# Performance work log

Measured on AMD Instinct MI355X. Metric: run time of the kernel, lower is better.

## Reference

```python
import jax, jax.numpy as jnp
import numpy as np

VOC = 50000; E = 300; HE = 512; HO = 1024; TN = 5; A = 256; L = 100; T = 48; B = 32
DIN = E + HO + E  # 1624 decoder lstm input
HD = HO           # decoder hidden size


def lstm_cell(x, h, c, Wih, Whh, b):
    g = x @ Wih.T + h @ Whh.T + b
    i, f, gg, o = jnp.split(g, 4, axis=-1)  # torch gate order i,f,g,o
    c2 = jax.nn.sigmoid(f) * c + jax.nn.sigmoid(i) * jnp.tanh(gg)
    h2 = jax.nn.sigmoid(o) * jnp.tanh(c2)
    return h2, c2


def run_lstm(xs, Wih, Whh, b, H):
    # xs: [S, B, E] seq-first
    h0 = jnp.zeros((xs.shape[1], H), xs.dtype)
    def step(carry, x):
        h, c = carry
        h2, c2 = lstm_cell(x, h, c, Wih, Whh, b)
        return (h2, c2), h2
    (h, c), ys = jax.lax.scan(step, (h0, h0), xs)
    return ys, h, c


def _forward(topics, essay, mems, enc_emb, enc_Wih_f, enc_Whh_f, enc_b_f,
             enc_Wih_b, enc_Whh_b, enc_b_b, dec_emb, dec_Wih, dec_Whh, dec_b,
             Wfc, bfc, mem_emb, Wm, bm, U1, bU1, V1, bV1, U2, bU2, V2, bV2,
             W1, b1, W2, b2, W3, b3):
    # ---- Encoder (bidirectional, 1 layer, all lengths == TN so pack/sort is identity)
    x = enc_emb[topics.T]                                  # [TN, B, E]
    ys_f, hf, cf = run_lstm(x, enc_Wih_f, enc_Whh_f, enc_b_f, HE)
    ys_b, hb, cb = run_lstm(x[::-1], enc_Wih_b, enc_Whh_b, enc_b_b, HE)
    topics_repr = jnp.concatenate([ys_f, ys_b[::-1]], axis=-1)  # [TN, B, 2*HE]
    # torch: h [2,B,HE] -> reshape(1,B,2*HE); replicate the row-major reshape exactly
    h0 = jnp.stack([hf, hb]).reshape(B, 2 * HE)
    c0 = jnp.stack([cf, cb]).reshape(B, 2 * HE)

    mem0 = mem_emb[mems]                                   # [B, L, E]

    def before_feed(emb_y, h_last, c_last, mem):
        # replicate the original (axis-mixing) reshapes faithfully (row-major, same as torch)
        pre = (topics_repr.reshape(B * TN, -1) @ W1.T + b1).reshape(B, TN, -1)  # [B,TN,A]
        q = (c_last @ W2.T + b2)[:, :, None]                                    # [B,A,1]
        e = jnp.tanh(pre @ q)[..., 0] @ W3.T + b3                               # [B,TN]
        alpha = jax.nn.softmax(e, axis=1)
        c_t = (topics_repr.reshape(B, -1, TN) @ alpha[:, :, None])[..., 0]      # [B,2*HE]
        # memory attention read
        v = jnp.tanh(h_last @ Wm.T + bm)                                        # [B,E]
        qm = jax.nn.softmax(mem @ v[:, :, None], axis=1)                        # [B,L,1]
        m = (jnp.swapaxes(qm, 1, 2) @ mem)[:, 0]                                # [B,E]
        return jnp.concatenate([emb_y, c_t, m], axis=1)                         # [B,DIN]

    def update_memory(mem, emb):
        Mt = jnp.tanh(mem @ U1.T + bU1 + (emb @ V1.T + bV1)[:, None])
        g = jax.nn.sigmoid(mem @ U2.T + bU2 + (emb @ V2.T + bV2)[:, None])
        return Mt * g + mem * (1.0 - g)

    emb0 = dec_emb[essay[:, 0]]                            # [B,E]
    dec_in0 = before_feed(emb0, h0, c0, mem0)

    # teacher forcing always: next token at step t is essay[:, t+1] (last is dummy/unused)
    next_toks = jnp.concatenate([essay[:, 1:], essay[:, -1:]], axis=1).T  # [T,B]

    def step(carry, tok):
        hh, cc, mem, dec_in = carry
        h1, c1 = lstm_cell(dec_in, hh, cc, dec_Wih, dec_Whh, dec_b)
        logits = h1 @ Wfc.T + bfc                          # [B,VOC]
        emb = dec_emb[tok]
        mem2 = update_memory(mem, emb)
        dec_in2 = before_feed(emb, h1, c1, mem2)
        return (h1, c1, mem2, dec_in2), logits

    _, logits_all = jax.lax.scan(step, (h0, c0, mem0, dec_in0), next_toks)
    return logits_all                                      # [T, B, VOC]


def setup_inputs():
    key = jax.random.key(0)
    ks = iter(jax.random.split(key, 48))
    def rn(shape, s=0.02):
        return (jax.random.normal(next(ks), shape) * s).astype(jnp.float32)
    return dict(
        topics=jax.random.randint(next(ks), (B, TN), 0, VOC),
        essay=jax.random.randint(next(ks), (B, T), 0, VOC),
        mems=jax.random.randint(next(ks), (B, L), 0, VOC),
        enc_emb=rn((VOC, E), 0.1),
        enc_Wih_f=rn((4 * HE, E)), enc_Whh_f=rn((4 * HE, HE)), enc_b_f=rn((4 * HE,)),
        enc_Wih_b=rn((4 * HE, E)), enc_Whh_b=rn((4 * HE, HE)), enc_b_b=rn((4 * HE,)),
        dec_emb=rn((VOC, E), 0.1),
        dec_Wih=rn((4 * HD, DIN)), dec_Whh=rn((4 * HD, HD)), dec_b=rn((4 * HD,)),
        Wfc=rn((VOC, HD)), bfc=rn((VOC,)),
        mem_emb=rn((VOC, E), 0.1),
        Wm=rn((E, HD)), bm=rn((E,)),
        U1=rn((E, E)), bU1=rn((E,)), V1=rn((E, E)), bV1=rn((E,)),
        U2=rn((E, E)), bU2=rn((E,)), V2=rn((E, E)), bV2=rn((E,)),
        W1=rn((A, 2 * HE)), b1=rn((A,)),
        W2=rn((A, HD)), b2=rn((A,)),
        W3=rn((TN, TN)), b3=rn((TN,)),
    )


def reference(topics, essay, mems, enc_emb, enc_Wih_f, enc_Whh_f, enc_b_f,
              enc_Wih_b, enc_Whh_b, enc_b_b, dec_emb, dec_Wih, dec_Whh, dec_b,
              Wfc, bfc, mem_emb, Wm, bm, U1, bU1, V1, bV1, U2, bU2, V2, bV2,
              W1, b1, W2, b2, W3, b3):
    return _forward(topics, essay, mems, enc_emb, enc_Wih_f, enc_Whh_f, enc_b_f,
                    enc_Wih_b, enc_Whh_b, enc_b_b, dec_emb, dec_Wih, dec_Whh, dec_b,
                    Wfc, bfc, mem_emb, Wm, bm, U1, bU1, V1, bV1, U2, bU2, V2, bV2,
                    W1, b1, W2, b2, W3, b3)
```

## Files before the change

kernel.cpp:

```cpp
#include <hip/hip_runtime.h>
#include <stdint.h>

typedef unsigned short u16;
typedef unsigned int   u32;
typedef __bf16 bf16v8 __attribute__((ext_vector_type(8)));
typedef float  f32x4  __attribute__((ext_vector_type(4)));

#define DEV static __device__ __forceinline__

DEV int imin(int a, int b){ return a < b ? a : b; }
DEV float bf2f(u16 u){ union{u32 i; float f;} v; v.i = ((u32)u) << 16; return v.f; }
DEV u16 f2bf(float f){ union{float f; u32 i;} v; v.f = f; return (u16)((v.i + 0x7fffu + ((v.i >> 16) & 1u)) >> 16); }
DEV float sigmf(float x){ return 1.0f / (1.0f + __expf(-x)); }
DEV float tanhf_(float x){ return 1.0f - 2.0f / (__expf(2.0f * x) + 1.0f); }

DEV bf16v8 ldb8(const u16* p){ return *reinterpret_cast<const bf16v8*>(p); }
#define MFMA16(a,b,c) __builtin_amdgcn_mfma_f32_16x16x32_bf16(a,b,c,0,0,0)

__global__ __launch_bounds__(256) void cvt_weights(
    const float* eWih_f, const float* eWih_b, const float* eWhh_f, const float* eWhh_b,
    const float* dWih, const float* dWhh,
    const float* U1, const float* U2, const float* V1, const float* V2,
    const float* W1, const float* W2, const float* Wm,
    u16* WihF_p, u16* WihB_p, u16* WhhF, u16* WhhB, u16* dWih_p, u16* dWhh16,
    u16* U1p, u16* U2p, u16* V1p, u16* V2p, u16* W1b, u16* W2b, u16* Wmp)
{
  int blk = blockIdx.x, tid = threadIdx.x;
  const float* src; u16* dst; int sw, dw, valid;
  if (blk < 2048)       { src = eWih_f + (size_t)blk * 300; dst = WihF_p + (size_t)blk * 320; sw = 300; dw = 320; valid = 1; }
  else if (blk < 4096)  { int r = blk - 2048;  src = eWih_b + (size_t)r * 300;  dst = WihB_p + (size_t)r * 320;  sw = 300;  dw = 320;  valid = 1; }
  else if (blk < 6144)  { int r = blk - 4096;  src = eWhh_f + (size_t)r * 512;  dst = WhhF  + (size_t)r * 512;  sw = 512;  dw = 512;  valid = 1; }
  else if (blk < 8192)  { int r = blk - 6144;  src = eWhh_b + (size_t)r * 512;  dst = WhhB  + (size_t)r * 512;  sw = 512;  dw = 512;  valid = 1; }
  else if (blk < 12288) { int r = blk - 8192;  src = dWih  + (size_t)r * 1624; dst = dWih_p + (size_t)r * 1632; sw = 1624; dw = 1632; valid = 1; }
  else if (blk < 16384) { int r = blk - 12288; src = dWhh  + (size_t)r * 1024; dst = dWhh16 + (size_t)r * 1024; sw = 1024; dw = 1024; valid = 1; }
  else if (blk < 16688) { int r = blk - 16384; src = U1 + (size_t)imin(r,299) * 300; dst = U1p + (size_t)r * 320; sw = 300; dw = 320; valid = (r < 300); }
  else if (blk < 16992) { int r = blk - 16688; src = U2 + (size_t)imin(r,299) * 300; dst = U2p + (size_t)r * 320; sw = 300; dw = 320; valid = (r < 300); }
  else if (blk < 17296) { int r = blk - 16992; src = V1 + (size_t)imin(r,299) * 300; dst = V1p + (size_t)r * 320; sw = 300; dw = 320; valid = (r < 300); }
  else if (blk < 17600) { int r = blk - 17296; src = V2 + (size_t)imin(r,299) * 300; dst = V2p + (size_t)r * 320; sw = 300; dw = 320; valid = (r < 300); }
  else if (blk < 17856) { int r = blk - 17600; src = W1 + (size_t)r * 1024; dst = W1b + (size_t)r * 1024; sw = 1024; dw = 1024; valid = 1; }
  else if (blk < 18112) { int r = blk - 17856; src = W2 + (size_t)r * 1024; dst = W2b + (size_t)r * 1024; sw = 1024; dw = 1024; valid = 1; }
  else                  { int r = blk - 18112; src = Wm + (size_t)imin(r,299) * 1024; dst = Wmp + (size_t)r * 1024; sw = 1024; dw = 1024; valid = (r < 300); }
  for (int i = tid; i < dw; i += 256) dst[i] = (valid && i < sw) ? f2bf(src[i]) : (u16)0;
}

__global__ __launch_bounds__(256) void gather_init(
    const int* topics, const int* essay, const int* mems,
    const float* enc_emb, const float* dec_emb, const float* mem_emb,
    u16* x_enc, u16* memb, u16* emb_seq, u16* emb0, u16* h_enc, float* c_enc)
{
  int blk = blockIdx.x, tid = threadIdx.x;
  if (blk < 160) {
    int t = blk / 32, b = blk % 32;
    int tok = topics[b * 5 + t];
    u16* dst = x_enc + (size_t)blk * 320;
    const float* src = enc_emb + (size_t)tok * 300;
    for (int i = tid; i < 320; i += 256) dst[i] = (i < 300) ? f2bf(src[i]) : (u16)0;
  } else if (blk < 3360) {
    int s = blk - 160;
    int tok = mems[s];
    u16* d0 = memb + (size_t)s * 320;
    u16* d1 = memb + (size_t)(3200 + s) * 320;
    const float* src = mem_emb + (size_t)tok * 300;
    for (int i = tid; i < 320; i += 256) { d0[i] = (i < 300) ? f2bf(src[i]) : (u16)0; d1[i] = 0; }
  } else if (blk < 4896) {
    int r = blk - 3360;
    int t = r / 32, b = r % 32;
    int tok = essay[b * 48 + (t < 47 ? t + 1 : 47)];
    u16* dst = emb_seq + (size_t)r * 320;
    const float* src = dec_emb + (size_t)tok * 300;
    for (int i = tid; i < 320; i += 256) dst[i] = (i < 300) ? f2bf(src[i]) : (u16)0;
  } else if (blk < 4928) {
    int b = blk - 4896;
    int tok = essay[b * 48];
    u16* dst = emb0 + (size_t)b * 320;
    const float* src = dec_emb + (size_t)tok * 300;
    for (int i = tid; i < 320; i += 256) dst[i] = (i < 300) ? f2bf(src[i]) : (u16)0;
  } else {
    int id = blk - 4928;
    if (id < 64) {
      int dir = id / 32, m = id % 32;
      u16* p = h_enc + ((size_t)(dir * 2 + 0) * 32 + m) * 512;
      for (int i = tid; i < 512; i += 256) p[i] = 0;
    } else {
      int id2 = id - 64;
      int dir = id2 / 32, m = id2 % 32;
      float* p = c_enc + ((size_t)(dir * 2 + 0) * 32 + m) * 512;
      for (int i = tid; i < 512; i += 256) p[i] = 0.0f;
    }
  }
}

__global__ __launch_bounds__(256) void vemb_gemm(
    const u16* emb_seq, const u16* V1p, const u16* V2p, const float* bV1, const float* bV2, float* vemb)
{
  int m0 = blockIdx.x * 32;
  int tid = threadIdx.x, w = tid >> 6, lane = tid & 63;
  int lr = lane & 15, lk = (lane >> 4) * 8;
  const u16* ur[10]; int cols[10];
  f32x4 acc0[10], acc1[10];
  #pragma unroll
  for (int i = 0; i < 10; ++i) {
    acc0[i] = (f32x4){0,0,0,0}; acc1[i] = (f32x4){0,0,0,0};
    int col = (w * 10 + i) * 16 + lr; cols[i] = col;
    if (col < 304)      ur[i] = V1p + (size_t)col * 320;
    else if (col < 608) ur[i] = V2p + (size_t)(col - 304) * 320;
    else                ur[i] = V1p;
  }
  for (int k0 = 0; k0 < 320; k0 += 32) {
    bf16v8 a0 = ldb8(emb_seq + (size_t)(m0 + lr) * 320 + k0 + lk);
    bf16v8 a1 = ldb8(emb_seq + (size_t)(m0 + 16 + lr) * 320 + k0 + lk);
    #pragma unroll
    for (int i = 0; i < 10; ++i) {
      bf16v8 b = ldb8(ur[i] + k0 + lk);
      acc0[i] = MFMA16(a0, b, acc0[i]);
      acc1[i] = MFMA16(a1, b, acc1[i]);
    }
  }
  int rb = (lane >> 4) * 4;
  #pragma unroll
  for (int i = 0; i < 10; ++i) {
    int col = cols[i];
    if (col >= 608) continue;
    float bb = (col < 304) ? ((col < 300) ? bV1[col] : 0.f) : ((col - 304 < 300) ? bV2[col - 304] : 0.f);
    #pragma unroll
    for (int r = 0; r < 4; ++r) {
      vemb[(size_t)(m0 + rb + r) * 608 + col]      = acc0[i][r] + bb;
      vemb[(size_t)(m0 + 16 + rb + r) * 608 + col] = acc1[i][r] + bb;
    }
  }
}

__global__ __launch_bounds__(256) void enc_step(
    int t, const u16* x_enc,
    const u16* WihF_p, const u16* WhhF, const float* b_f,
    const u16* WihB_p, const u16* WhhB, const float* b_b,
    u16* h_enc, float* c_enc, float* ys_f, float* ys_b)
{
  int blk = blockIdx.x, tid = threadIdx.x;
  int dir = blk >> 5, jb = blk & 31, j0 = jb * 16;
  int w = tid >> 6, lane = tid & 63, lr = lane & 15, lk = (lane >> 4) * 8;
  const u16* Wih = dir ? WihB_p : WihF_p;
  const u16* Whh = dir ? WhhB : WhhF;
  const float* bias = dir ? b_b : b_f;
  const u16* xrow = x_enc + (size_t)(dir ? (4 - t) : t) * 32 * 320;
  const u16* h_prev = h_enc + ((size_t)(dir * 2 + (t & 1)) * 32) * 512;
  u16* h_next = h_enc + ((size_t)(dir * 2 + ((t + 1) & 1)) * 32) * 512;
  const float* c_prev = c_enc + ((size_t)(dir * 2 + (t & 1)) * 32) * 512;
  float* c_next = c_enc + ((size_t)(dir * 2 + ((t + 1) & 1)) * 32) * 512;
  float* ys = (dir ? ys_b : ys_f) + (size_t)t * 32 * 512;

  int wrow = w * 512 + j0 + lr;
  f32x4 acc0 = {0,0,0,0}, acc1 = {0,0,0,0};
  const u16* bp1 = Wih + (size_t)wrow * 320;
  #pragma unroll 2
  for (int k0 = 0; k0 < 320; k0 += 32) {
    bf16v8 b = ldb8(bp1 + k0 + lk);
    bf16v8 a0 = ldb8(xrow + (size_t)lr * 320 + k0 + lk);
    bf16v8 a1 = ldb8(xrow + (size_t)(lr + 16) * 320 + k0 + lk);
    acc0 = MFMA16(a0, b, acc0); acc1 = MFMA16(a1, b, acc1);
  }
  const u16* bp2 = Whh + (size_t)wrow * 512;
  #pragma unroll 4
  for (int k0 = 0; k0 < 512; k0 += 32) {
    bf16v8 b = ldb8(bp2 + k0 + lk);
    bf16v8 a0 = ldb8(h_prev + (size_t)lr * 512 + k0 + lk);
    bf16v8 a1 = ldb8(h_prev + (size_t)(lr + 16) * 512 + k0 + lk);
    acc0 = MFMA16(a0, b, acc0); acc1 = MFMA16(a1, b, acc1);
  }
  float bb = bias[wrow];
  __shared__ float lg[4][32][16];
  int rb = (lane >> 4) * 4;
  #pragma unroll
  for (int r = 0; r < 4; ++r) {
    lg[w][rb + r][lr] = acc0[r] + bb;
    lg[w][16 + rb + r][lr] = acc1[r] + bb;
  }
  __syncthreads();
  for (int i = tid; i < 512; i += 256) {
    int m = i >> 4, jj = i & 15, col = j0 + jj;
    float ig = lg[0][m][jj], fg = lg[1][m][jj], gg = lg[2][m][jj], og = lg[3][m][jj];
    float c_old = c_prev[(size_t)m * 512 + col];
    float c2 = sigmf(fg) * c_old + sigmf(ig) * tanhf_(gg);
    float h2 = sigmf(og) * tanhf_(c2);
    c_next[(size_t)m * 512 + col] = c2;
    h_next[(size_t)m * 512 + col] = f2bf(h2);
    ys[(size_t)m * 512 + col] = h2;
  }
}

__global__ __launch_bounds__(256) void prep_kernel(
    const float* ys_f, const float* ys_b, const float* c_enc,
    u16* h_pp, float* c_pp, u16* c_bfpp, float* TR_CT, u16* tr_pre)
{
  int blk = blockIdx.x, tid = threadIdx.x;
  if (blk < 32) {
    int r = blk;
    for (int c = tid; c < 1024; c += 256) {
      int bs = 2 * (r & 15) + (c >> 9), k = c & 511;
      const float* ysX = (r < 16) ? ys_f : ys_b;
      float hv = ysX[((size_t)4 * 32 + bs) * 512 + k];
      float cv = c_enc[((size_t)(((r < 16) ? 0 : 1) * 2 + 1) * 32 + bs) * 512 + k];
      h_pp[(size_t)r * 1024 + c] = f2bf(hv);
      c_pp[(size_t)r * 1024 + c] = cv;
      c_bfpp[(size_t)r * 1024 + c] = f2bf(cv);
    }
  } else if (blk < 64) {
    int b2 = blk - 32;
    for (int i = tid; i < 5120; i += 256) {
      int f = b2 * 5120 + i;
      int tt = f >> 15, bb = (f >> 10) & 31, dd = f & 1023;
      float v = (dd < 512) ? ys_f[((size_t)tt * 32 + bb) * 512 + dd]
                           : ys_b[((size_t)(4 - tt) * 32 + bb) * 512 + (dd - 512)];
      TR_CT[(size_t)b2 * 5120 + i] = v;
    }
  } else {
    int i = blk - 64;
    int st = i >> 5, sb = i & 31;
    for (int c = tid; c < 1024; c += 256) {
      float v = (c < 512) ? ys_f[((size_t)st * 32 + sb) * 512 + c]
                          : ys_b[((size_t)(4 - st) * 32 + sb) * 512 + (c - 512)];
      tr_pre[(size_t)i * 1024 + c] = f2bf(v);
    }
  }
}

__global__ __launch_bounds__(64) void pre_gemm(const u16* tr_pre, const u16* W1b, const float* b1, float* pre)
{
  int blk = blockIdx.x, mt = blk >> 4, nt = blk & 15;
  int lane = threadIdx.x & 63, lr = lane & 15, lk = (lane >> 4) * 8;
  int col = nt * 16 + lr;
  f32x4 acc = {0,0,0,0};
  const u16* brow = W1b + (size_t)col * 1024;
  const u16* arow = tr_pre + (size_t)(mt * 16 + lr) * 1024;
  #pragma unroll 4
  for (int k0 = 0; k0 < 1024; k0 += 32)
    acc = MFMA16(ldb8(arow + k0 + lk), ldb8(brow + k0 + lk), acc);
  float bb = b1[col];
  int rb = (lane >> 4) * 4;
  #pragma unroll
  for (int r = 0; r < 4; ++r)
    pre[(size_t)(mt * 16 + rb + r) * 256 + col] = acc[r] + bb;
}

__global__ __launch_bounds__(256) void dec_stepA(
    int t, const u16* dec_in, const u16* dWih_p, const u16* dWhh16, const float* dbias,
    u16* h_pp, float* c_pp, u16* c_bfpp, u16* h_seq,
    u16* memb, const u16* U1p, const u16* U2p, const float* bU1, const float* bU2, const float* vemb)
{
  int blk = blockIdx.x, tid = threadIdx.x;
  int w = tid >> 6, lane = tid & 63, lr = lane & 15, lk = (lane >> 4) * 8;
  __shared__ float lg[4][32][16];
  if (blk < 64) {
    int j0 = blk * 16;
    const u16* h_prev = h_pp + (size_t)(t & 1) * 32768;
    u16* h_next = h_pp + (size_t)((t + 1) & 1) * 32768;
    const float* c_prev = c_pp + (size_t)(t & 1) * 32768;
    float* c_next = c_pp + (size_t)((t + 1) & 1) * 32768;
    u16* cb_next = c_bfpp + (size_t)((t + 1) & 1) * 32768;
    int wrow = w * 1024 + j0 + lr;
    f32x4 acc0 = {0,0,0,0}, acc1 = {0,0,0,0};
    const u16* bp1 = dWih_p + (size_t)wrow * 1632;
    #pragma unroll 4
    for (int k0 = 0; k0 < 1632; k0 += 32) {
      bf16v8 b = ldb8(bp1 + k0 + lk);
      bf16v8 a0 = ldb8(dec_in + (size_t)lr * 1632 + k0 + lk);
      bf16v8 a1 = ldb8(dec_in + (size_t)(lr + 16) * 1632 + k0 + lk);
      acc0 = MFMA16(a0, b, acc0); acc1 = MFMA16(a1, b, acc1);
    }
    const u16* bp2 = dWhh16 + (size_t)wrow * 1024;
    #pragma unroll 4
    for (int k0 = 0; k0 < 1024; k0 += 32) {
      bf16v8 b = ldb8(bp2 + k0 + lk);
      bf16v8 a0 = ldb8(h_prev + (size_t)lr * 1024 + k0 + lk);
      bf16v8 a1 = ldb8(h_prev + (size_t)(lr + 16) * 1024 + k0 + lk);
      acc0 = MFMA16(a0, b, acc0); acc1 = MFMA16(a1, b, acc1);
    }
    float bb = dbias[wrow];
    int rb = (lane >> 4) * 4;
    #pragma unroll
    for (int r = 0; r < 4; ++r) {
      lg[w][rb + r][lr] = acc0[r] + bb;
      lg[w][16 + rb + r][lr] = acc1[r] + bb;
    }
    __syncthreads();
    for (int i = tid; i < 512; i += 256) {
      int m = i >> 4, jj = i & 15, col = j0 + jj;
      float ig = lg[0][m][jj], fg = lg[1][m][jj], gg = lg[2][m][jj], og = lg[3][m][jj];
      float c_old = c_prev[(size_t)m * 1024 + col];
      float c2 = sigmf(fg) * c_old + sigmf(ig) * tanhf_(gg);
      float h2 = sigmf(og) * tanhf_(c2);
      c_next[(size_t)m * 1024 + col] = c2;
      cb_next[(size_t)m * 1024 + col] = f2bf(c2);
      h_next[(size_t)m * 1024 + col] = f2bf(h2);
      h_seq[((size_t)t * 32 + m) * 1024 + col] = f2bf(h2);
    }
  } else {
    if (t == 47) return;
    int s0 = (blk - 64) * 32;
    const u16* mcur = memb + (size_t)(t & 1) * 3200 * 320;
    u16* mnext = memb + (size_t)((t + 1) & 1) * 3200 * 320;
    int jt0 = w * 5, njt = (w == 3) ? 4 : 5;
    f32x4 accA[2][5], accB[2][5];
    const u16 *r1[5], *r2[5];
    #pragma unroll
    for (int i = 0; i < 5; ++i) {
      accA[0][i] = (f32x4){0,0,0,0}; accA[1][i] = (f32x4){0,0,0,0};
      accB[0][i] = (f32x4){0,0,0,0}; accB[1][i] = (f32x4){0,0,0,0};
      int col = (jt0 + i) * 16 + lr; int cc = imin(col, 303);
      r1[i] = U1p + (size_t)cc * 320; r2[i] = U2p + (size_t)cc * 320;
    }
    for (int k0 = 0; k0 < 320; k0 += 32) {
      bf16v8 a0 = ldb8(mcur + (size_t)(s0 + lr) * 320 + k0 + lk);
      bf16v8 a1 = ldb8(mcur + (size_t)(s0 + 16 + lr) * 320 + k0 + lk);
      #pragma unroll
      for (int i = 0; i < 5; ++i) {
        if (i < njt) {
          bf16v8 b1v = ldb8(r1[i] + k0 + lk);
          bf16v8 b2v = ldb8(r2[i] + k0 + lk);
          accA[0][i] = MFMA16(a0, b1v, accA[0][i]);
          accA[1][i] = MFMA16(a1, b1v, accA[1][i]);
          accB[0][i] = MFMA16(a0, b2v, accB[0][i]);
          accB[1][i] = MFMA16(a1, b2v, accB[1][i]);
        }
      }
    }
    int rb = (lane >> 4) * 4;
    #pragma unroll
    for (int i = 0; i < 5; ++i) {
      if (i >= njt) break;
      int col = (jt0 + i) * 16 + lr;
      if (col >= 300) continue;
      float bu1 = bU1[col], bu2 = bU2[col];
      #pragma unroll
      for (int mt = 0; mt < 2; ++mt) {
        #pragma unroll
        for (int r = 0; r < 4; ++r) {
          int slot = s0 + mt * 16 + rb + r;
          int bb = slot / 100;
          const float* vrow = vemb + ((size_t)t * 32 + bb) * 608;
          float mtp = (mt ? accA[1][i][r] : accA[0][i][r]) + bu1 + vrow[col];
          float gp  = (mt ? accB[1][i][r] : accB[0][i][r]) + bu2 + vrow[304 + col];
          float old = bf2f(mcur[(size_t)slot * 320 + col]);
          float g = sigmf(gp);
          mnext[(size_t)slot * 320 + col] = f2bf(tanhf_(mtp) * g + old * (1.0f - g));
        }
      }
    }
  }
}

__global__ __launch_bounds__(64) void dec_stepB1(
    int t, const u16* h_pp, const u16* c_bfpp,
    const u16* W2b, const float* b2, const u16* Wmp, const float* bm,
    float* q_all, float* v_all)
{
  int blk = blockIdx.x, lane = threadIdx.x & 63;
  int lr = lane & 15, lk = (lane >> 4) * 8;
  int pp = (t + 1) & 1;
  const u16* h = h_pp + (size_t)pp * 32768;
  const u16* c = c_bfpp + (size_t)pp * 32768;
  f32x4 acc0 = {0,0,0,0}, acc1 = {0,0,0,0};
  int rb = (lane >> 4) * 4;
  if (blk < 16) {
    int col = blk * 16 + lr;
    const u16* brow = W2b + (size_t)col * 1024;
    #pragma unroll 4
    for (int k0 = 0; k0 < 1024; k0 += 32) {
      bf16v8 b = ldb8(brow + k0 + lk);
      acc0 = MFMA16(ldb8(c + (size_t)lr * 1024 + k0 + lk), b, acc0);
      acc1 = MFMA16(ldb8(c + (size_t)(lr + 16) * 1024 + k0 + lk), b, acc1);
    }
    float bb = b2[col];
    #pragma unroll
    for (int r = 0; r < 4; ++r) {
      q_all[(size_t)(rb + r) * 256 + col] = acc0[r] + bb;
      q_all[(size_t)(16 + rb + r) * 256 + col] = acc1[r] + bb;
    }
  } else {
    int col = (blk - 16) * 16 + lr;
    const u16* brow = Wmp + (size_t)imin(col, 303) * 1024;
    #pragma unroll 4
    for (int k0 = 0; k0 < 1024; k0 += 32) {
      bf16v8 b = ldb8(brow + k0 + lk);
      acc0 = MFMA16(ldb8(h + (size_t)lr * 1024 + k0 + lk), b, acc0);
      acc1 = MFMA16(ldb8(h + (size_t)(lr + 16) * 1024 + k0 + lk), b, acc1);
    }
    if (col < 300) {
      float bb = bm[col];
      #pragma unroll
      for (int r = 0; r < 4; ++r) {
        v_all[(size_t)(rb + r) * 304 + col] = tanhf_(acc0[r] + bb);
        v_all[(size_t)(16 + rb + r) * 304 + col] = tanhf_(acc1[r] + bb);
      }
    }
  }
}

__global__ __launch_bounds__(256) void dec_stepB2(
    int t, const float* q_all, const float* v_all, const float* pre,
    const float* W3, const float* b3, const float* TR_CT,
    const u16* memb, const u16* emb_seq, const u16* emb0, u16* dec_in)
{
  int b = blockIdx.x, tid = threadIdx.x;
  __shared__ float sq[256], red[256], se[5], salpha[5], sv[304], ssc[100], sqm[100], ssum[2];
  const u16* mrow = memb + (size_t)((t + 1) & 1) * 3200 * 320 + (size_t)b * 100 * 320;
  const u16* erow = (t < 0) ? (emb0 + (size_t)b * 320) : (emb_seq + ((size_t)t * 32 + b) * 320);
  u16* drow = dec_in + (size_t)b * 1632;

  sq[tid] = q_all[(size_t)b * 256 + tid];
  __syncthreads();
  for (int tn = 0; tn < 5; ++tn) {
    red[tid] = pre[((size_t)b * 5 + tn) * 256 + tid] * sq[tid];
    __syncthreads();
    for (int s = 128; s > 0; s >>= 1) { if (tid < s) red[tid] += red[tid + s]; __syncthreads(); }
    if (tid == 0) se[tn] = tanhf_(red[0]);
    __syncthreads();
  }
  if (tid == 0) {
    float e2[5]; float mx = -1e30f;
    for (int j = 0; j < 5; ++j) {
      float s = b3[j];
      for (int tn = 0; tn < 5; ++tn) s += se[tn] * W3[j * 5 + tn];
      e2[j] = s; mx = fmaxf(mx, s);
    }
    float sum = 0.f;
    for (int j = 0; j < 5; ++j) { e2[j] = __expf(e2[j] - mx); sum += e2[j]; }
    float inv = 1.f / sum;
    for (int j = 0; j < 5; ++j) salpha[j] = e2[j] * inv;
  }
  __syncthreads();
  for (int d = tid; d < 1024; d += 256) {
    const float* tc = TR_CT + ((size_t)b * 1024 + d) * 5;
    float ct = tc[0]*salpha[0] + tc[1]*salpha[1] + tc[2]*salpha[2] + tc[3]*salpha[3] + tc[4]*salpha[4];
    drow[300 + d] = f2bf(ct);
  }
  for (int i = tid; i < 304; i += 256) sv[i] = (i < 300) ? v_all[(size_t)b * 304 + i] : 0.f;
  __syncthreads();
  if (tid < 100) {
    const u16* mr = mrow + (size_t)tid * 320;
    float s = 0.f;
    for (int e = 0; e < 300; ++e) s += bf2f(mr[e]) * sv[e];
    ssc[tid] = s;
  }
  __syncthreads();
  if (tid == 0) { float mx = -1e30f; for (int l = 0; l < 100; ++l) mx = fmaxf(mx, ssc[l]); ssum[0] = mx; }
  __syncthreads();
  if (tid < 100) sqm[tid] = __expf(ssc[tid] - ssum[0]);
  __syncthreads();
  if (tid == 0) { float s = 0.f; for (int l = 0; l < 100; ++l) s += sqm[l]; ssum[1] = 1.f / s; }
  __syncthreads();
  float inv = ssum[1];
  for (int e = tid; e < 300; e += 256) {
    float acc = 0.f;
    for (int l = 0; l < 100; ++l) acc += sqm[l] * bf2f(mrow[(size_t)l * 320 + e]);
    drow[1324 + e] = f2bf(acc * inv);
    drow[e] = erow[e];
  }
  if (tid < 8) drow[1624 + tid] = 0;
}

__global__ __launch_bounds__(256) void logits_gemm(
    const u16* h_seq, const float* Wfc, const float* bfc, float* out)
{
  __shared__ u16 As[128 * 40], Bs[128 * 40];
  int tid = threadIdx.x;
  int n0 = blockIdx.x * 128, m0 = blockIdx.y * 128;
  int w = tid >> 6, lane = tid & 63, lr = lane & 15, lk = (lane >> 4) * 8;
  int wr = w >> 1, wc = w & 1;
  int sr = tid >> 1, sc = (tid & 1) * 16;
  const u16* ga = h_seq + (size_t)(m0 + sr) * 1024 + sc;
  int brow = n0 + sr; if (brow > 49999) brow = 49999;
  const float* gb = Wfc + (size_t)brow * 1024 + sc;
  f32x4 acc[4][4];
  #pragma unroll
  for (int i = 0; i < 4; ++i)
    #pragma unroll
    for (int j = 0; j < 4; ++j) acc[i][j] = (f32x4){0,0,0,0};

  bf16v8 pa0 = ldb8(ga), pa1 = ldb8(ga + 8);
  float4 qb0 = *(const float4*)(gb), qb1 = *(const float4*)(gb + 4);
  float4 qb2 = *(const float4*)(gb + 8), qb3 = *(const float4*)(gb + 12);
  for (int kt = 0; kt < 32; ++kt) {
    __syncthreads();
    *reinterpret_cast<bf16v8*>(&As[sr * 40 + sc]) = pa0;
    *reinterpret_cast<bf16v8*>(&As[sr * 40 + sc + 8]) = pa1;
    u16* bd = &Bs[sr * 40 + sc];
    bd[0] = f2bf(qb0.x); bd[1] = f2bf(qb0.y); bd[2] = f2bf(qb0.z); bd[3] = f2bf(qb0.w);
    bd[4] = f2bf(qb1.x); bd[5] = f2bf(qb1.y); bd[6] = f2bf(qb1.z); bd[7] = f2bf(qb1.w);
    bd[8] = f2bf(qb2.x); bd[9] = f2bf(qb2.y); bd[10] = f2bf(qb2.z); bd[11] = f2bf(qb2.w);
    bd[12] = f2bf(qb3.x); bd[13] = f2bf(qb3.y); bd[14] = f2bf(qb3.z); bd[15] = f2bf(qb3.w);
    __syncthreads();
    if (kt < 31) {
      int k = (kt + 1) * 32;
      pa0 = ldb8(ga + k); pa1 = ldb8(ga + k + 8);
      qb0 = *(const float4*)(gb + k); qb1 = *(const float4*)(gb + k + 4);
      qb2 = *(const float4*)(gb + k + 8); qb3 = *(const float4*)(gb + k + 12);
    }
    bf16v8 af[4], bf[4];
    #pragma unroll
    for (int mi = 0; mi < 4; ++mi)
      af[mi] = *reinterpret_cast<const bf16v8*>(&As[(wr * 64 + mi * 16 + lr) * 40 + lk]);
    #pragma unroll
    for (int ni = 0; ni < 4; ++ni)
      bf[ni] = *reinterpret_cast<const bf16v8*>(&Bs[(wc * 64 + ni * 16 + lr) * 40 + lk]);
    #pragma unroll
    for (int mi = 0; mi < 4; ++mi)
      #pragma unroll
      for (int ni = 0; ni < 4; ++ni)
        acc[mi][ni] = MFMA16(af[mi], bf[ni], acc[mi][ni]);
  }
  int rb = (lane >> 4) * 4;
  #pragma unroll
  for (int mi = 0; mi < 4; ++mi) {
    #pragma unroll
    for (int ni = 0; ni < 4; ++ni) {
      int col = n0 + wc * 64 + ni * 16 + lr;
      if (col < 50000) {
        float bb = bfc[col];
        int row = m0 + wr * 64 + mi * 16 + rb;
        #pragma unroll
        for (int r = 0; r < 4; ++r)
          out[(size_t)(row + r) * 50000 + col] = acc[mi][ni][r] + bb;
      }
    }
  }
}

extern "C" void kernel_launch(void* const* d_in, const int* in_sizes, int n_in,
                              void* d_out, int out_size, void* d_ws, size_t ws_size,
                              hipStream_t stream)
{
  (void)in_sizes; (void)n_in; (void)out_size; (void)ws_size;
  const int* topics = (const int*)d_in[0];
  const int* essay  = (const int*)d_in[1];
  const int* mems   = (const int*)d_in[2];
  const float* enc_emb = (const float*)d_in[3];
  const float* eWih_f = (const float*)d_in[4];
  const float* eWhh_f = (const float*)d_in[5];
  const float* eb_f   = (const float*)d_in[6];
  const float* eWih_b = (const float*)d_in[7];
  const float* eWhh_b = (const float*)d_in[8];
  const float* eb_b   = (const float*)d_in[9];
  const float* dec_emb = (const float*)d_in[10];
  const float* dWih   = (const float*)d_in[11];
  const float* dWhh   = (const float*)d_in[12];
  const float* db_    = (const float*)d_in[13];
  const float* Wfc    = (const float*)d_in[14];
  const float* bfc    = (const float*)d_in[15];
  const float* mem_emb = (const float*)d_in[16];
  const float* Wm     = (const float*)d_in[17];
  const float* bm     = (const float*)d_in[18];
  const float* U1     = (const float*)d_in[19];
  const float* bU1    = (const float*)d_in[20];
  const float* V1     = (const float*)d_in[21];
  const float* bV1    = (const float*)d_in[22];
  const float* U2     = (const float*)d_in[23];
  const float* bU2    = (const float*)d_in[24];
  const float* V2     = (const float*)d_in[25];
  const float* bV2    = (const float*)d_in[26];
  const float* W1     = (const float*)d_in[27];
  const float* b1     = (const float*)d_in[28];
  const float* W2     = (const float*)d_in[29];
  const float* b2     = (const float*)d_in[30];
  const float* W3     = (const float*)d_in[31];
  const float* b3     = (const float*)d_in[32];

  char* ws = (char*)d_ws;
  size_t off = 0;
  auto alloc = [&](size_t bytes) -> char* {
    char* p = ws + off; off += (bytes + 255) & ~(size_t)255; return p;
  };
  float* ys_f  = (float*)alloc((size_t)5*32*512*4);
  float* ys_b  = (float*)alloc((size_t)5*32*512*4);
  float* c_enc = (float*)alloc((size_t)2*2*32*512*4);
  float* c_pp  = (float*)alloc((size_t)2*32*1024*4);
  float* TR_CT = (float*)alloc((size_t)32*1024*5*4);
  float* pre   = (float*)alloc((size_t)160*256*4);
  float* vemb  = (float*)alloc((size_t)1536*608*4);
  float* q_all = (float*)alloc((size_t)32*256*4);
  float* v_all = (float*)alloc((size_t)32*304*4);
  u16* x_enc   = (u16*)alloc((size_t)160*320*2);
  u16* emb_seq = (u16*)alloc((size_t)1536*320*2);
  u16* emb0    = (u16*)alloc((size_t)32*320*2);
  u16* memb    = (u16*)alloc((size_t)2*3200*320*2);
  u16* h_enc   = (u16*)alloc((size_t)2*2*32*512*2);
  u16* h_pp    = (u16*)alloc((size_t)2*32*1024*2);
  u16* c_bfpp  = (u16*)alloc((size_t)2*32*1024*2);
  u16* dec_in  = (u16*)alloc((size_t)32*1632*2);
  u16* tr_pre  = (u16*)alloc((size_t)160*1024*2);
  u16* h_seq   = (u16*)alloc((size_t)1536*1024*2);
  u16* WihF_p  = (u16*)alloc((size_t)2048*320*2);
  u16* WihB_p  = (u16*)alloc((size_t)2048*320*2);
  u16* WhhF    = (u16*)alloc((size_t)2048*512*2);
  u16* WhhB    = (u16*)alloc((size_t)2048*512*2);
  u16* dWih_p  = (u16*)alloc((size_t)4096*1632*2);
  u16* dWhh16  = (u16*)alloc((size_t)4096*1024*2);
  u16* U1p     = (u16*)alloc((size_t)304*320*2);
  u16* U2p     = (u16*)alloc((size_t)304*320*2);
  u16* V1p     = (u16*)alloc((size_t)304*320*2);
  u16* V2p     = (u16*)alloc((size_t)304*320*2);
  u16* W1b     = (u16*)alloc((size_t)256*1024*2);
  u16* W2b     = (u16*)alloc((size_t)256*1024*2);
  u16* Wmp     = (u16*)alloc((size_t)304*1024*2);
  float* out   = (float*)d_out;

  cvt_weights<<<18416, 256, 0, stream>>>(eWih_f, eWih_b, eWhh_f, eWhh_b, dWih, dWhh,
                                         U1, U2, V1, V2, W1, W2, Wm,
                                         WihF_p, WihB_p, WhhF, WhhB, dWih_p, dWhh16,
                                         U1p, U2p, V1p, V2p, W1b, W2b, Wmp);
  gather_init<<<5056, 256, 0, stream>>>(topics, essay, mems, enc_emb, dec_emb, mem_emb,
                                        x_enc, memb, emb_seq, emb0, h_enc, c_enc);
  vemb_gemm<<<48, 256, 0, stream>>>(emb_seq, V1p, V2p, bV1, bV2, vemb);
  for (int t = 0; t < 5; ++t)
    enc_step<<<64, 256, 0, stream>>>(t, x_enc, WihF_p, WhhF, eb_f, WihB_p, WhhB, eb_b,
                                     h_enc, c_enc, ys_f, ys_b);
  prep_kernel<<<224, 256, 0, stream>>>(ys_f, ys_b, c_enc, h_pp, c_pp, c_bfpp, TR_CT, tr_pre);
  pre_gemm<<<160, 64, 0, stream>>>(tr_pre, W1b, b1, pre);
  dec_stepB1<<<35, 64, 0, stream>>>(-1, h_pp, c_bfpp, W2b, b2, Wmp, bm, q_all, v_all);
  dec_stepB2<<<32, 256, 0, stream>>>(-1, q_all, v_all, pre, W3, b3, TR_CT, memb, emb_seq, emb0, dec_in);
  for (int t = 0; t < 48; ++t) {
    dec_stepA<<<164, 256, 0, stream>>>(t, dec_in, dWih_p, dWhh16, db_, h_pp, c_pp, c_bfpp, h_seq,
                                       memb, U1p, U2p, bU1, bU2, vemb);
    if (t < 47) {
      dec_stepB1<<<35, 64, 0, stream>>>(t, h_pp, c_bfpp, W2b, b2, Wmp, bm, q_all, v_all);
      dec_stepB2<<<32, 256, 0, stream>>>(t, q_all, v_all, pre, W3, b3, TR_CT, memb, emb_seq, emb0, dec_in);
    }
  }
  logits_gemm<<<dim3(391, 12), 256, 0, stream>>>(h_seq, Wfc, bfc, out);
}
```

Measured before the change: 3.533 ms.

## Fuse decoder time loop into persistent kernel with grid barriers; XCD-remap logits GEMM

Replaces the 48-step loop of three kernel launches per step with one persistent 64-block kernel that runs LSTM, projection/memory update and attention phases, separated by atomic-counter grid barriers. This removes about 140 launches and their gaps on the serial critical path. The memory-update work that used to run on 100 extra blocks concurrently is now spread over 64 blocks, and each barrier adds spin latency. The logits GEMM also gets a 1D grid with block IDs remapped so that each XCD works on contiguous tiles, which is meant to improve L2 reuse.

```diff
diff --git a/kernel.cpp b/kernel.cpp
--- a/kernel.cpp
+++ b/kernel.cpp
@@ -16,6 +16,26 @@
 
 DEV bf16v8 ldb8(const u16* p){ return *reinterpret_cast<const bf16v8*>(p); }
 #define MFMA16(a,b,c) __builtin_amdgcn_mfma_f32_16x16x32_bf16(a,b,c,0,0,0)
+
+#define NBLK 64
+
+DEV void gbar(int* cnt, int* gen) {
+  __syncthreads();
+  if (threadIdx.x == 0) {
+    __threadfence();
+    int g = __hip_atomic_load(gen, __ATOMIC_RELAXED, __HIP_MEMORY_SCOPE_AGENT);
+    int prev = __hip_atomic_fetch_add(cnt, 1, __ATOMIC_ACQ_REL, __HIP_MEMORY_SCOPE_AGENT);
+    if (prev == NBLK - 1) {
+      __hip_atomic_store(cnt, 0, __ATOMIC_RELAXED, __HIP_MEMORY_SCOPE_AGENT);
+      __hip_atomic_store(gen, g + 1, __ATOMIC_RELEASE, __HIP_MEMORY_SCOPE_AGENT);
+    } else {
+      while (__hip_atomic_load(gen, __ATOMIC_ACQUIRE, __HIP_MEMORY_SCOPE_AGENT) == g)
+        __builtin_amdgcn_s_sleep(2);
+    }
+    __threadfence();
+  }
+  __syncthreads();
+}
 
 __global__ __launch_bounds__(256) void cvt_weights(
     const float* eWih_f, const float* eWih_b, const float* eWhh_f, const float* eWhh_b,
@@ -23,9 +43,10 @@
     const float* U1, const float* U2, const float* V1, const float* V2,
     const float* W1, const float* W2, const float* Wm,
     u16* WihF_p, u16* WihB_p, u16* WhhF, u16* WhhB, u16* dWih_p, u16* dWhh16,
-    u16* U1p, u16* U2p, u16* V1p, u16* V2p, u16* W1b, u16* W2b, u16* Wmp)
+    u16* U1p, u16* U2p, u16* V1p, u16* V2p, u16* W1b, u16* W2b, u16* Wmp, int* syncp)
 {
   int blk = blockIdx.x, tid = threadIdx.x;
+  if (blk == 0 && tid < 2) syncp[tid * 64] = 0;
   const float* src; u16* dst; int sw, dw, valid;
   if (blk < 2048)       { src = eWih_f + (size_t)blk * 300; dst = WihF_p + (size_t)blk * 320; sw = 300; dw = 320; valid = 1; }
   else if (blk < 4096)  { int r = blk - 2048;  src = eWih_b + (size_t)r * 300;  dst = WihB_p + (size_t)r * 320;  sw = 300;  dw = 320;  valid = 1; }
@@ -242,116 +263,9 @@
     pre[(size_t)(mt * 16 + rb + r) * 256 + col] = acc[r] + bb;
 }
 
-__global__ __launch_bounds__(256) void dec_stepA(
-    int t, const u16* dec_in, const u16* dWih_p, const u16* dWhh16, const float* dbias,
-    u16* h_pp, float* c_pp, u16* c_bfpp, u16* h_seq,
-    u16* memb, const u16* U1p, const u16* U2p, const float* bU1, const float* bU2, const float* vemb)
-{
-  int blk = blockIdx.x, tid = threadIdx.x;
-  int w = tid >> 6, lane = tid & 63, lr = lane & 15, lk = (lane >> 4) * 8;
-  __shared__ float lg[4][32][16];
-  if (blk < 64) {
-    int j0 = blk * 16;
-    const u16* h_prev = h_pp + (size_t)(t & 1) * 32768;
-    u16* h_next = h_pp + (size_t)((t + 1) & 1) * 32768;
-    const float* c_prev = c_pp + (size_t)(t & 1) * 32768;
-    float* c_next = c_pp + (size_t)((t + 1) & 1) * 32768;
-    u16* cb_next = c_bfpp + (size_t)((t + 1) & 1) * 32768;
-    int wrow = w * 1024 + j0 + lr;
-    f32x4 acc0 = {0,0,0,0}, acc1 = {0,0,0,0};
-    const u16* bp1 = dWih_p + (size_t)wrow * 1632;
-    #pragma unroll 4
-    for (int k0 = 0; k0 < 1632; k0 += 32) {
-      bf16v8 b = ldb8(bp1 + k0 + lk);
-      bf16v8 a0 = ldb8(dec_in + (size_t)lr * 1632 + k0 + lk);
-      bf16v8 a1 = ldb8(dec_in + (size_t)(lr + 16) * 1632 + k0 + lk);
-      acc0 = MFMA16(a0, b, acc0); acc1 = MFMA16(a1, b, acc1);
-    }
-    const u16* bp2 = dWhh16 + (size_t)wrow * 1024;
-    #pragma unroll 4
-    for (int k0 = 0; k0 < 1024; k0 += 32) {
-      bf16v8 b = ldb8(bp2 + k0 + lk);
-      bf16v8 a0 = ldb8(h_prev + (size_t)lr * 1024 + k0 + lk);
-      bf16v8 a1 = ldb8(h_prev + (size_t)(lr + 16) * 1024 + k0 + lk);
-      acc0 = MFMA16(a0, b, acc0); acc1 = MFMA16(a1, b, acc1);
-    }
-    float bb = dbias[wrow];
-    int rb = (lane >> 4) * 4;
-    #pragma unroll
-    for (int r = 0; r < 4; ++r) {
-      lg[w][rb + r][lr] = acc0[r] + bb;
-      lg[w][16 + rb + r][lr] = acc1[r] + bb;
-    }
-    __syncthreads();
-    for (int i = tid; i < 512; i += 256) {
-      int m = i >> 4, jj = i & 15, col = j0 + jj;
-      float ig = lg[0][m][jj], fg = lg[1][m][jj], gg = lg[2][m][jj], og = lg[3][m][jj];
-      float c_old = c_prev[(size_t)m * 1024 + col];
-      float c2 = sigmf(fg) * c_old + sigmf(ig) * tanhf_(gg);
-      float h2 = sigmf(og) * tanhf_(c2);
-      c_next[(size_t)m * 1024 + col] = c2;
-      cb_next[(size_t)m * 1024 + col] = f2bf(c2);
-      h_next[(size_t)m * 1024 + col] = f2bf(h2);
-      h_seq[((size_t)t * 32 + m) * 1024 + col] = f2bf(h2);
-    }
-  } else {
-    if (t == 47) return;
-    int s0 = (blk - 64) * 32;
-    const u16* mcur = memb + (size_t)(t & 1) * 3200 * 320;
-    u16* mnext = memb + (size_t)((t + 1) & 1) * 3200 * 320;
-    int jt0 = w * 5, njt = (w == 3) ? 4 : 5;
-    f32x4 accA[2][5], accB[2][5];
-    const u16 *r1[5], *r2[5];
-    #pragma unroll
-    for (int i = 0; i < 5; ++i) {
-      accA[0][i] = (f32x4){0,0,0,0}; accA[1][i] = (f32x4){0,0,0,0};
-      accB[0][i] = (f32x4){0,0,0,0}; accB[1][i] = (f32x4){0,0,0,0};
-      int col = (jt0 + i) * 16 + lr; int cc = imin(col, 303);
-      r1[i] = U1p + (size_t)cc * 320; r2[i] = U2p + (size_t)cc * 320;
-    }
-    for (int k0 = 0; k0 < 320; k0 += 32) {
-      bf16v8 a0 = ldb8(mcur + (size_t)(s0 + lr) * 320 + k0 + lk);
-      bf16v8 a1 = ldb8(mcur + (size_t)(s0 + 16 + lr) * 320 + k0 + lk);
-      #pragma unroll
-      for (int i = 0; i < 5; ++i) {
-        if (i < njt) {
-          bf16v8 b1v = ldb8(r1[i] + k0 + lk);
-          bf16v8 b2v = ldb8(r2[i] + k0 + lk);
-          accA[0][i] = MFMA16(a0, b1v, accA[0][i]);
-          accA[1][i] = MFMA16(a1, b1v, accA[1][i]);
-          accB[0][i] = MFMA16(a0, b2v, accB[0][i]);
-          accB[1][i] = MFMA16(a1, b2v, accB[1][i]);
-        }
-      }
-    }
-    int rb = (lane >> 4) * 4;
-    #pragma unroll
-    for (int i = 0; i < 5; ++i) {
-      if (i >= njt) break;
-      int col = (jt0 + i) * 16 + lr;
-      if (col >= 300) continue;
-      float bu1 = bU1[col], bu2 = bU2[col];
-      #pragma unroll
-      for (int mt = 0; mt < 2; ++mt) {
-        #pragma unroll
-        for (int r = 0; r < 4; ++r) {
-          int slot = s0 + mt * 16 + rb + r;
-          int bb = slot / 100;
-          const float* vrow = vemb + ((size_t)t * 32 + bb) * 608;
-          float mtp = (mt ? accA[1][i][r] : accA[0][i][r]) + bu1 + vrow[col];
-          float gp  = (mt ? accB[1][i][r] : accB[0][i][r]) + bu2 + vrow[304 + col];
-          float old = bf2f(mcur[(size_t)slot * 320 + col]);
-          float g = sigmf(gp);
-          mnext[(size_t)slot * 320 + col] = f2bf(tanhf_(mtp) * g + old * (1.0f - g));
-        }
-      }
-    }
-  }
-}
-
 __global__ __launch_bounds__(64) void dec_stepB1(
     int t, const u16* h_pp, const u16* c_bfpp,
-    const u16* W2b, const float* b2, const u16* Wmp, const float* bm,
+    const u16* W2b, const float* bias2, const u16* Wmp, const float* biasm,
     float* q_all, float* v_all)
 {
   int blk = blockIdx.x, lane = threadIdx.x & 63;
@@ -370,7 +284,7 @@
       acc0 = MFMA16(ldb8(c + (size_t)lr * 1024 + k0 + lk), b, acc0);
       acc1 = MFMA16(ldb8(c + (size_t)(lr + 16) * 1024 + k0 + lk), b, acc1);
     }
-    float bb = b2[col];
+    float bb = bias2[col];
     #pragma unroll
     for (int r = 0; r < 4; ++r) {
       q_all[(size_t)(rb + r) * 256 + col] = acc0[r] + bb;
@@ -386,7 +300,7 @@
       acc1 = MFMA16(ldb8(h + (size_t)(lr + 16) * 1024 + k0 + lk), b, acc1);
     }
     if (col < 300) {
-      float bb = bm[col];
+      float bb = biasm[col];
       #pragma unroll
       for (int r = 0; r < 4; ++r) {
         v_all[(size_t)(rb + r) * 304 + col] = tanhf_(acc0[r] + bb);
@@ -459,12 +373,237 @@
   if (tid < 8) drow[1624 + tid] = 0;
 }
 
+__global__ __launch_bounds__(256, 1) void dec_persistent(
+    const u16* dWih_p, const u16* dWhh16, const float* dbias,
+    u16* dec_in, u16* h_pp, float* c_pp, u16* c_bfpp, u16* h_seq,
+    u16* memb, const u16* U1p, const u16* U2p, const float* bU1, const float* bU2, const float* vemb,
+    const u16* W2b, const float* bias2, const u16* Wmp, const float* biasm,
+    float* q_all, float* v_all, const float* pre, const float* W3, const float* b3,
+    const float* TR_CT, const u16* emb_seq, int* syncp)
+{
+  int blk = blockIdx.x, tid = threadIdx.x;
+  int w = tid >> 6, lane = tid & 63, lr = lane & 15, lk = (lane >> 4) * 8;
+  int* cnt = syncp; int* gen = syncp + 64;
+  __shared__ float lg[4][32][16];
+  __shared__ float sq[256], red[256], se[5], salpha[5], sv[304], ssc[100], sqm[100], ssum[2];
+
+  for (int t = 0; t < 48; ++t) {
+    {
+      int j0 = blk * 16;
+      const u16* h_prev = h_pp + (size_t)(t & 1) * 32768;
+      u16* h_next = h_pp + (size_t)((t + 1) & 1) * 32768;
+      const float* c_prev = c_pp + (size_t)(t & 1) * 32768;
+      float* c_next = c_pp + (size_t)((t + 1) & 1) * 32768;
+      u16* cb_next = c_bfpp + (size_t)((t + 1) & 1) * 32768;
+      int wrow = w * 1024 + j0 + lr;
+      f32x4 acc0 = {0,0,0,0}, acc1 = {0,0,0,0};
+      const u16* bp1 = dWih_p + (size_t)wrow * 1632;
+      #pragma unroll 4
+      for (int k0 = 0; k0 < 1632; k0 += 32) {
+        bf16v8 b = ldb8(bp1 + k0 + lk);
+        bf16v8 a0 = ldb8(dec_in + (size_t)lr * 1632 + k0 + lk);
+        bf16v8 a1 = ldb8(dec_in + (size_t)(lr + 16) * 1632 + k0 + lk);
+        acc0 = MFMA16(a0, b, acc0); acc1 = MFMA16(a1, b, acc1);
+      }
+      const u16* bp2 = dWhh16 + (size_t)wrow * 1024;
+      #pragma unroll 4
+      for (int k0 = 0; k0 < 1024; k0 += 32) {
+        bf16v8 b = ldb8(bp2 + k0 + lk);
+        bf16v8 a0 = ldb8(h_prev + (size_t)lr * 1024 + k0 + lk);
+        bf16v8 a1 = ldb8(h_prev + (size_t)(lr + 16) * 1024 + k0 + lk);
+        acc0 = MFMA16(a0, b, acc0); acc1 = MFMA16(a1, b, acc1);
+      }
+      float bb = dbias[wrow];
+      int rb = (lane >> 4) * 4;
+      #pragma unroll
+      for (int r = 0; r < 4; ++r) {
+        lg[w][rb + r][lr] = acc0[r] + bb;
+        lg[w][16 + rb + r][lr] = acc1[r] + bb;
+      }
+      __syncthreads();
+      for (int i = tid; i < 512; i += 256) {
+        int m = i >> 4, jj = i & 15, col = j0 + jj;
+        float ig = lg[0][m][jj], fg = lg[1][m][jj], gg = lg[2][m][jj], og = lg[3][m][jj];
+        float c_old = c_prev[(size_t)m * 1024 + col];
+        float c2 = sigmf(fg) * c_old + sigmf(ig) * tanhf_(gg);
+        float h2 = sigmf(og) * tanhf_(c2);
+        c_next[(size_t)m * 1024 + col] = c2;
+        cb_next[(size_t)m * 1024 + col] = f2bf(c2);
+        h_next[(size_t)m * 1024 + col] = f2bf(h2);
+        h_seq[((size_t)t * 32 + m) * 1024 + col] = f2bf(h2);
+      }
+    }
+    if (t == 47) break;
+    gbar(cnt, gen);
+
+    {
+      int wid = blk * 4 + w;
+      int pp = (t + 1) & 1;
+      if (wid < 35) {
+        const u16* h = h_pp + (size_t)pp * 32768;
+        const u16* c = c_bfpp + (size_t)pp * 32768;
+        f32x4 acc0 = {0,0,0,0}, acc1 = {0,0,0,0};
+        int rb = (lane >> 4) * 4;
+        if (wid < 16) {
+          int col = wid * 16 + lr;
+          const u16* brow = W2b + (size_t)col * 1024;
+          #pragma unroll 4
+          for (int k0 = 0; k0 < 1024; k0 += 32) {
+            bf16v8 b = ldb8(brow + k0 + lk);
+            acc0 = MFMA16(ldb8(c + (size_t)lr * 1024 + k0 + lk), b, acc0);
+            acc1 = MFMA16(ldb8(c + (size_t)(lr + 16) * 1024 + k0 + lk), b, acc1);
+          }
+          float bb = bias2[col];
+          #pragma unroll
+          for (int r = 0; r < 4; ++r) {
+            q_all[(size_t)(rb + r) * 256 + col] = acc0[r] + bb;
+            q_all[(size_t)(16 + rb + r) * 256 + col] = acc1[r] + bb;
+          }
+        } else {
+          int col = (wid - 16) * 16 + lr;
+          const u16* brow = Wmp + (size_t)imin(col, 303) * 1024;
+          #pragma unroll 4
+          for (int k0 = 0; k0 < 1024; k0 += 32) {
+            bf16v8 b = ldb8(brow + k0 + lk);
+            acc0 = MFMA16(ldb8(h + (size_t)lr * 1024 + k0 + lk), b, acc0);
+            acc1 = MFMA16(ldb8(h + (size_t)(lr + 16) * 1024 + k0 + lk), b, acc1);
+          }
+          if (col < 300) {
+            float bb = biasm[col];
+            #pragma unroll
+            for (int r = 0; r < 4; ++r) {
+              v_all[(size_t)(rb + r) * 304 + col] = tanhf_(acc0[r] + bb);
+              v_all[(size_t)(16 + rb + r) * 304 + col] = tanhf_(acc1[r] + bb);
+            }
+          }
+        }
+      }
+      const u16* mcur = memb + (size_t)(t & 1) * 3200 * 320;
+      u16* mnext = memb + (size_t)((t + 1) & 1) * 3200 * 320;
+      for (int mt2 = blk; mt2 < 100; mt2 += NBLK) {
+        int s0 = mt2 * 32;
+        int jt0 = w * 5, njt = (w == 3) ? 4 : 5;
+        f32x4 accA[2][5], accB[2][5];
+        const u16 *r1[5], *r2[5];
+        #pragma unroll
+        for (int i = 0; i < 5; ++i) {
+          accA[0][i] = (f32x4){0,0,0,0}; accA[1][i] = (f32x4){0,0,0,0};
+          accB[0][i] = (f32x4){0,0,0,0}; accB[1][i] = (f32x4){0,0,0,0};
+          int col = (jt0 + i) * 16 + lr; int cc = imin(col, 303);
+          r1[i] = U1p + (size_t)cc * 320; r2[i] = U2p + (size_t)cc * 320;
+        }
+        for (int k0 = 0; k0 < 320; k0 += 32) {
+          bf16v8 a0 = ldb8(mcur + (size_t)(s0 + lr) * 320 + k0 + lk);
+          bf16v8 a1 = ldb8(mcur + (size_t)(s0 + 16 + lr) * 320 + k0 + lk);
+          #pragma unroll
+          for (int i = 0; i < 5; ++i) {
+            if (i < njt) {
+              bf16v8 b1v = ldb8(r1[i] + k0 + lk);
+              bf16v8 b2v = ldb8(r2[i] + k0 + lk);
+              accA[0][i] = MFMA16(a0, b1v, accA[0][i]);
+              accA[1][i] = MFMA16(a1, b1v, accA[1][i]);
+              accB[0][i] = MFMA16(a0, b2v, accB[0][i]);
+              accB[1][i] = MFMA16(a1, b2v, accB[1][i]);
+            }
+          }
+        }
+        int rb = (lane >> 4) * 4;
+        #pragma unroll
+        for (int i = 0; i < 5; ++i) {
+          if (i >= njt) break;
+          int col = (jt0 + i) * 16 + lr;
+          if (col >= 300) continue;
+          float bu1 = bU1[col], bu2 = bU2[col];
+          #pragma unroll
+          for (int mh = 0; mh < 2; ++mh) {
+            #pragma unroll
+            for (int r = 0; r < 4; ++r) {
+              int slot = s0 + mh * 16 + rb + r;
+              int bb = slot / 100;
+              const float* vrow = vemb + ((size_t)t * 32 + bb) * 608;
+              float mtp = (mh ? accA[1][i][r] : accA[0][i][r]) + bu1 + vrow[col];
+              float gp  = (mh ? accB[1][i][r] : accB[0][i][r]) + bu2 + vrow[304 + col];
+              float old = bf2f(mcur[(size_t)slot * 320 + col]);
+              float g = sigmf(gp);
+              mnext[(size_t)slot * 320 + col] = f2bf(tanhf_(mtp) * g + old * (1.0f - g));
+            }
+          }
+        }
+      }
+    }
+    gbar(cnt, gen);
+
+    if (blk < 32) {
+      int b = blk;
+      const u16* mrow = memb + (size_t)((t + 1) & 1) * 3200 * 320 + (size_t)b * 100 * 320;
+      const u16* erow = emb_seq + ((size_t)t * 32 + b) * 320;
+      u16* drow = dec_in + (size_t)b * 1632;
+      sq[tid] = q_all[(size_t)b * 256 + tid];
+      __syncthreads();
+      for (int tn = 0; tn < 5; ++tn) {
+        red[tid] = pre[((size_t)b * 5 + tn) * 256 + tid] * sq[tid];
+        __syncthreads();
+        for (int s = 128; s > 0; s >>= 1) { if (tid < s) red[tid] += red[tid + s]; __syncthreads(); }
+        if (tid == 0) se[tn] = tanhf_(red[0]);
+        __syncthreads();
+      }
+      if (tid == 0) {
+        float e2[5]; float mx = -1e30f;
+        for (int j = 0; j < 5; ++j) {
+          float s = b3[j];
+          for (int tn = 0; tn < 5; ++tn) s += se[tn] * W3[j * 5 + tn];
+          e2[j] = s; mx = fmaxf(mx, s);
+        }
+        float sum = 0.f;
+        for (int j = 0; j < 5; ++j) { e2[j] = __expf(e2[j] - mx); sum += e2[j]; }
+        float inv = 1.f / sum;
+        for (int j = 0; j < 5; ++j) salpha[j] = e2[j] * inv;
+      }
+      __syncthreads();
+      for (int d = tid; d < 1024; d += 256) {
+        const float* tc = TR_CT + ((size_t)b * 1024 + d) * 5;
+        float ct = tc[0]*salpha[0] + tc[1]*salpha[1] + tc[2]*salpha[2] + tc[3]*salpha[3] + tc[4]*salpha[4];
+        drow[300 + d] = f2bf(ct);
+      }
+      for (int i = tid; i < 304; i += 256) sv[i] = (i < 300) ? v_all[(size_t)b * 304 + i] : 0.f;
+      __syncthreads();
+      if (tid < 100) {
+        const u16* mr = mrow + (size_t)tid * 320;
+        float s = 0.f;
+        for (int e = 0; e < 300; ++e) s += bf2f(mr[e]) * sv[e];
+        ssc[tid] = s;
+      }
+      __syncthreads();
+      if (tid == 0) { float mx = -1e30f; for (int l = 0; l < 100; ++l) mx = fmaxf(mx, ssc[l]); ssum[0] = mx; }
+      __syncthreads();
+      if (tid < 100) sqm[tid] = __expf(ssc[tid] - ssum[0]);
+      __syncthreads();
+      if (tid == 0) { float s = 0.f; for (int l = 0; l < 100; ++l) s += sqm[l]; ssum[1] = 1.f / s; }
+      __syncthreads();
+      float inv = ssum[1];
+      for (int e = tid; e < 300; e += 256) {
+        float acc = 0.f;
+        for (int l = 0; l < 100; ++l) acc += sqm[l] * bf2f(mrow[(size_t)l * 320 + e]);
+        drow[1324 + e] = f2bf(acc * inv);
+        drow[e] = erow[e];
+      }
+      if (tid < 8) drow[1624 + tid] = 0;
+    }
+    gbar(cnt, gen);
+  }
+}
+
 __global__ __launch_bounds__(256) void logits_gemm(
     const u16* h_seq, const float* Wfc, const float* bfc, float* out)
 {
+  int id = blockIdx.x;
+  const int NW = 4692, qc = NW / 8, rc = NW % 8;
+  int xcd = id & 7, rank = id >> 3;
+  int work = (xcd < rc ? xcd * (qc + 1) : rc * (qc + 1) + (xcd - rc) * qc) + rank;
+  int n0 = (work / 12) * 128, m0 = (work % 12) * 128;
+
   __shared__ u16 As[128 * 40], Bs[128 * 40];
   int tid = threadIdx.x;
-  int n0 = blockIdx.x * 128, m0 = blockIdx.y * 128;
   int w = tid >> 6, lane = tid & 63, lr = lane & 15, lk = (lane >> 4) * 8;
   int wr = w >> 1, wc = w & 1;
   int sr = tid >> 1, sc = (tid & 1) * 16;
@@ -602,12 +741,13 @@
   u16* W1b     = (u16*)alloc((size_t)256*1024*2);
   u16* W2b     = (u16*)alloc((size_t)256*1024*2);
   u16* Wmp     = (u16*)alloc((size_t)304*1024*2);
+  int* syncp   = (int*)alloc((size_t)256*4);
   float* out   = (float*)d_out;
 
   cvt_weights<<<18416, 256, 0, stream>>>(eWih_f, eWih_b, eWhh_f, eWhh_b, dWih, dWhh,
                                          U1, U2, V1, V2, W1, W2, Wm,
                                          WihF_p, WihB_p, WhhF, WhhB, dWih_p, dWhh16,
-                                         U1p, U2p, V1p, V2p, W1b, W2b, Wmp);
+                                         U1p, U2p, V1p, V2p, W1b, W2b, Wmp, syncp);
   gather_init<<<5056, 256, 0, stream>>>(topics, essay, mems, enc_emb, dec_emb, mem_emb,
                                         x_enc, memb, emb_seq, emb0, h_enc, c_enc);
   vemb_gemm<<<48, 256, 0, stream>>>(emb_seq, V1p, V2p, bV1, bV2, vemb);
@@ -618,13 +758,11 @@
   pre_gemm<<<160, 64, 0, stream>>>(tr_pre, W1b, b1, pre);
   dec_stepB1<<<35, 64, 0, stream>>>(-1, h_pp, c_bfpp, W2b, b2, Wmp, bm, q_all, v_all);
   dec_stepB2<<<32, 256, 0, stream>>>(-1, q_all, v_all, pre, W3, b3, TR_CT, memb, emb_seq, emb0, dec_in);
-  for (int t = 0; t < 48; ++t) {
-    dec_stepA<<<164, 256, 0, stream>>>(t, dec_in, dWih_p, dWhh16, db_, h_pp, c_pp, c_bfpp, h_seq,
-                                       memb, U1p, U2p, bU1, bU2, vemb);
-    if (t < 47) {
-      dec_stepB1<<<35, 64, 0, stream>>>(t, h_pp, c_bfpp, W2b, b2, Wmp, bm, q_all, v_all);
-      dec_stepB2<<<32, 256, 0, stream>>>(t, q_all, v_all, pre, W3, b3, TR_CT, memb, emb_seq, emb0, dec_in);
-    }
-  }
-  logits_gemm<<<dim3(391, 12), 256, 0, stream>>>(h_seq, Wfc, bfc, out);
-}
+  dec_persistent<<<NBLK, 256, 0, stream>>>(dWih_p, dWhh16, db_,
+                                           dec_in, h_pp, c_pp, c_bfpp, h_seq,
+                                           memb, U1p, U2p, bU1, bU2, vemb,
+                                           W2b, b2, Wmp, bm,
+                                           q_all, v_all, pre, W3, b3,
+                                           TR_CT, emb_seq, syncp);
+  logits_gemm<<<4692, 256, 0, stream>>>(h_seq, Wfc, bfc, out);
+}
```

Measured after the change: 7.882 ms. 123% more time.
